# Performance work log

Measured on AMD Instinct MI355X. Metric: run time of the kernel, lower is better.

## Reference

```python
import jax, jax.numpy as jnp
import numpy as np

B = 16          # number of trees (batch)
H = 256         # hidden_size == feature_size
S = 16          # Tree.num_sem
C = 5           # max_child_num (complete C-ary tree)
L = 6           # tree depth: leaves at level L, internal levels 0..L-1
N_LEAF = C**L                     # 15625
N_INT = (C**L - 1) // (C - 1)     # 3906 internal nodes, level-l offset = (C^l-1)/(C-1)


def setup_inputs() -> dict:
    key = jax.random.key(0)
    ks = jax.random.split(key, 20)
    rn = lambda k, shp, s=0.05: jax.random.normal(k, shp, dtype=jnp.float32) * s
    return {
        "leaf_box": jax.random.normal(ks[0], (B, N_LEAF, 4), dtype=jnp.float32),
        "leaf_sem": jax.random.uniform(ks[1], (B, N_LEAF, S), dtype=jnp.float32),
        "internal_box": jax.random.normal(ks[2], (B, N_INT, 4), dtype=jnp.float32),
        "node_type": jax.random.randint(ks[3], (B, N_INT), 0, 3, dtype=jnp.int32),
        "eps": jax.random.normal(ks[4], (B, H), dtype=jnp.float32),
        "W_box": rn(ks[5], (4, H)), "b_box": jnp.zeros((H,), jnp.float32),
        "W_sem": rn(ks[6], (S, H)), "b_sem": jnp.zeros((H,), jnp.float32),
        "W_node": rn(ks[7], (3, C * H, H)), "b_node": jnp.zeros((3, H), jnp.float32),
        "W1": rn(ks[8], (H, H)), "b1": jnp.zeros((H,), jnp.float32),
        "Wmu": rn(ks[9], (H, H)), "bmu": jnp.zeros((H,), jnp.float32),
        "Wvar": rn(ks[10], (H, H)), "bvar": jnp.zeros((H,), jnp.float32),
    }


def reference(leaf_box, leaf_sem, internal_box, node_type, eps,
              W_box, b_box, W_sem, b_sem, W_node, b_node,
              W1, b1, Wmu, bmu, Wvar, bvar):
    box_enc = lambda b: jax.nn.relu(b @ W_box + b_box)
    # LeafEncoder: relu-box-encoding + relu-sem-encoding
    feats = box_enc(leaf_box) + jax.nn.relu(leaf_sem @ W_sem + b_sem)  # [B, N_LEAF, H]
    # Bottom-up over internal levels (static loop over L=6 levels)
    for l in range(L - 1, -1, -1):
        n = C ** l
        off = (C ** l - 1) // (C - 1)
        child = feats.reshape(B, n, C * H)  # children flattened per parent (child_exists==1)
        # Apply all 3 branch encoders (vertical/horizontal/stack), select by node label
        y_all = jnp.einsum('bnk,tkh->bnth', child, W_node) + b_node          # [B,n,3,H]
        sel = jax.nn.one_hot(node_type[:, off:off + n], 3, dtype=child.dtype)  # [B,n,3]
        y = jnp.einsum('bnth,bnt->bnh', y_all, sel)
        feats = jax.nn.relu(y) + box_enc(internal_box[:, off:off + n])
    root = feats[:, 0]  # [B, H]
    # Sampler (variational, probabilistic)
    enc = jax.nn.relu(root @ W1 + b1)
    mu = enc @ Wmu + bmu
    logvar = enc @ Wvar + bvar
    std = jnp.exp(0.5 * logvar)
    kld = 1.0 + logvar - mu ** 2 - jnp.exp(logvar)
    return jnp.concatenate([eps * std + mu, kld], axis=1)  # [B, 2H]
```

## Files before the change

kernel.cpp:

```cpp
#include <hip/hip_runtime.h>


#define B_ 16
#define H_ 256
#define NLEAF 15625
#define NINT 3906
#define RND128(x) (((x) + 127) & ~127)

typedef __bf16 bf16_t;
typedef bf16_t bf16x8 __attribute__((ext_vector_type(8)));
typedef bf16_t bf16x4 __attribute__((ext_vector_type(4)));
typedef float f32x4 __attribute__((ext_vector_type(4)));

__device__ __forceinline__ void gl2lds16(const bf16_t* g, bf16_t* l) {
  __builtin_amdgcn_global_load_lds((const __attribute__((address_space(1))) void*)g,
                                   (__attribute__((address_space(3))) void*)l,
                                   16, 0, 0);
}

__global__ __launch_bounds__(256) void prep_kernel(const float* __restrict__ W_node,
                                                   bf16_t* __restrict__ Wt,
                                                   int* __restrict__ counters) {
  if (blockIdx.x == 0 && threadIdx.x < 18) counters[threadIdx.x] = 0;
  const int t = blockIdx.x / 80;
  const int kc = blockIdx.x % 80;
  const int h = threadIdx.x;
  const int half = h >> 7, r = h & 127;
  const int sw = (r >> 1) & 3;
  const float* srcp = W_node + (size_t)t * 1280 * 256 + h;
  bf16_t* base = Wt + ((size_t)(t * 2 + half) * 40) * 4096 + r * 32;
#pragma unroll
  for (int k0 = kc * 16; k0 < kc * 16 + 16; k0 += 8) {
    bf16x8 v;
#pragma unroll
    for (int j = 0; j < 8; ++j) v[j] = (bf16_t)srcp[(size_t)(k0 + j) * 256];
    const int ks = k0 >> 5;
    const int q = (k0 >> 3) & 3;
    *(bf16x8*)(base + (size_t)ks * 4096 + ((q ^ sw) << 3)) = v;
  }
}

__global__ __launch_bounds__(256) void bucket_kernel(const int* __restrict__ node_type,
                                                     int* __restrict__ counters,
                                                     int2* __restrict__ buckets) {
  __shared__ int lcnt[18];
  __shared__ int lbase[18];
  const int tid = threadIdx.x;
  if (tid < 18) lcnt[tid] = 0;
  __syncthreads();

  int idx = blockIdx.x * 256 + tid;
  bool active = idx < B_ * NINT;
  int t = 0, key = 0, mypos = 0;
  int2 e;
  int base = 0, nl_cap = 0;
  if (active) {
    int b = idx / NINT;
    int j = idx - b * NINT;
    int l, off;
    if (j >= 781)      { l = 5; off = 781; }
    else if (j >= 156) { l = 4; off = 156; }
    else if (j >= 31)  { l = 3; off = 31; }
    else if (j >= 6)   { l = 2; off = 6; }
    else if (j >= 1)   { l = 1; off = 1; }
    else               { l = 0; off = 0; }
    const int n_tab[6]    = {1, 5, 25, 125, 625, 3125};
    const int nn_tab[6]   = {5, 25, 125, 625, 3125, 15625};
    const int base_tab[6] = {0, 48, 288, 1488, 7488, 37488};
    int n_l = n_tab[l], nn = nn_tab[l];
    t = node_type[idx];
    int i = j - off;
    e.x = b * n_l + i;
    e.y = b * nn + 5 * i;
    base = base_tab[l];
    nl_cap = B_ * n_l;
    key = l * 3 + t;
    mypos = atomicAdd(&lcnt[key], 1);
  }
  __syncthreads();
  if (tid < 18) {
    int c = lcnt[tid];
    lbase[tid] = c ? atomicAdd(&counters[tid], c) : 0;
  }
  __syncthreads();
  if (active) {
    buckets[base + t * nl_cap + lbase[key] + mypos] = e;
  }
}

__global__ __launch_bounds__(256) void dest_kernel(const int2* __restrict__ buckets,
                                                   const int* __restrict__ counters,
                                                   int* __restrict__ wdest_all,
                                                   int* __restrict__ rsrc6) {
  int flat = blockIdx.x * 256 + threadIdx.x;
  if (flat >= 187488) return;
  int l, base, cap, coff;
  if (flat >= 37488)      { l = 5; base = 37488; cap = 50000; coff = 0; }
  else if (flat >= 7488)  { l = 4; base = 7488;  cap = 10000; coff = 12480; }
  else if (flat >= 1488)  { l = 3; base = 1488;  cap = 2000;  coff = 2480; }
  else if (flat >= 288)   { l = 2; base = 288;   cap = 400;   coff = 480; }
  else if (flat >= 48)    { l = 1; base = 48;    cap = 80;    coff = 80; }
  else                    { l = 0; base = 0;     cap = 16;    coff = 0; }
  int rel = flat - base;
  int t = (rel >= 2 * cap) ? 2 : (rel >= cap ? 1 : 0);
  int s = rel - t * cap;
  const int* c3 = counters + l * 3;
  if (s >= c3[t]) return;
  int pfxr = (t > 0 ? RND128(c3[0]) : 0) + (t > 1 ? RND128(c3[1]) : 0);
  int R = pfxr + s;
  int2 e = buckets[flat];
  if (l == 5) {
    int* rp = rsrc6 + 5 * R;
#pragma unroll
    for (int c = 0; c < 5; ++c) rp[c] = e.y + c;
  } else {
    int* wp = wdest_all + coff + 5 * e.x;
#pragma unroll
    for (int c = 0; c < 5; ++c) wp[c] = (R << 3) + c;
  }
}

__global__ __launch_bounds__(256) void leaf_kernel(
    const float* __restrict__ leaf_box, const float* __restrict__ leaf_sem,
    const float* __restrict__ W_box, const float* __restrict__ b_box,
    const float* __restrict__ W_sem, const float* __restrict__ b_sem,
    const int* __restrict__ rsrc, bf16_t* __restrict__ g5) {
  const int lane = threadIdx.x & 63;
  const int wave = threadIdx.x >> 6;
  const int q = lane >> 4;
  const int c = lane & 15;
  const int hh = wave & 1;
  const int gw = wave >> 1;

  bf16x8 wsem[8], wbox[8];
#pragma unroll
  for (int T = 0; T < 8; ++T) {
    const int hb = (hh * 8 + T) * 16 + c;
    bf16x8 a;
#pragma unroll
    for (int j = 0; j < 8; ++j) a[j] = (bf16_t)0.f;
    if (q < 2) {
#pragma unroll
      for (int j = 0; j < 8; ++j) a[j] = (bf16_t)W_sem[(q * 8 + j) * H_ + hb];
    } else if (q == 2) {
      a[0] = (bf16_t)b_sem[hb];
    }
    wsem[T] = a;
    bf16x8 b;
#pragma unroll
    for (int j = 0; j < 8; ++j) b[j] = (bf16_t)0.f;
    if (q == 0) {
#pragma unroll
      for (int j = 0; j < 4; ++j) b[j] = (bf16_t)W_box[j * H_ + hb];
      b[4] = (bf16_t)b_box[hb];
    }
    wbox[T] = b;
  }

  const int NG2 = 15705;
  const int gstride = gridDim.x * 2;
  for (int g = blockIdx.x * 2 + gw; g < NG2; g += gstride) {
    const int ci = g * 16 + c;
    int row = rsrc[ci];
    row = ((unsigned)row < (unsigned)(B_ * NLEAF)) ? row : 0;
    const int R = ci / 5;
    const int c5 = ci - R * 5;
    bf16x8 xs, xb;
#pragma unroll
    for (int j = 0; j < 8; ++j) { xs[j] = (bf16_t)0.f; xb[j] = (bf16_t)0.f; }
    if (q < 2) {
      const float4* sp = (const float4*)(leaf_sem + (size_t)row * 16 + q * 8);
      float4 s0 = sp[0], s1 = sp[1];
      xs[0] = (bf16_t)s0.x; xs[1] = (bf16_t)s0.y; xs[2] = (bf16_t)s0.z; xs[3] = (bf16_t)s0.w;
      xs[4] = (bf16_t)s1.x; xs[5] = (bf16_t)s1.y; xs[6] = (bf16_t)s1.z; xs[7] = (bf16_t)s1.w;
    } else if (q == 2) {
      xs[0] = (bf16_t)1.0f;
    }
    if (q == 0) {
      float4 bx = *(const float4*)(leaf_box + (size_t)row * 4);
      xb[0] = (bf16_t)bx.x; xb[1] = (bf16_t)bx.y; xb[2] = (bf16_t)bx.z; xb[3] = (bf16_t)bx.w;
      xb[4] = (bf16_t)1.0f;
    }
    const int rr = R & 127;
    const int sw = (rr >> 1) & 3;
    bf16_t* obase = g5 + (size_t)(R >> 7) * 163840 + rr * 32;
#pragma unroll
    for (int T = 0; T < 8; ++T) {
      f32x4 z = {0.f, 0.f, 0.f, 0.f};
      f32x4 as = __builtin_amdgcn_mfma_f32_16x16x32_bf16(wsem[T], xs, z, 0, 0, 0);
      f32x4 ab = __builtin_amdgcn_mfma_f32_16x16x32_bf16(wbox[T], xb, z, 0, 0, 0);
      bf16x4 o;
#pragma unroll
      for (int r = 0; r < 4; ++r)
        o[r] = (bf16_t)(fmaxf(as[r], 0.f) + fmaxf(ab[r], 0.f));
      const int ks = c5 * 8 + hh * 4 + (T >> 1);
      const int pc = (((T & 1) << 1) | (q >> 1)) ^ sw;
      *(bf16x4*)(obase + (size_t)ks * 4096 + (pc << 3) + ((q & 1) << 2)) = o;
    }
  }
}

__global__ __launch_bounds__(256) void level_kernel(
    const bf16_t* __restrict__ src, bf16_t* __restrict__ dst,
    const int2* __restrict__ bucket, const int* __restrict__ counters,
    const bf16_t* __restrict__ Wt, const float* __restrict__ b_node,
    const float* __restrict__ ibox, const float* __restrict__ W_box,
    const float* __restrict__ b_box, const int* __restrict__ wdest,
    int n_l, int off_l, int cap) {
  const int t = blockIdx.y;
  const int cnt = counters[t];
  const int tile0 = blockIdx.x * 128;
  if (tile0 >= cnt) return;
  const int pfxr = (t > 0 ? RND128(counters[0]) : 0) + (t > 1 ? RND128(counters[1]) : 0);
  const int nblk = blockIdx.z;
  const int2* rd = bucket + (size_t)t * cap;

  __shared__ __align__(16) bf16_t Asm[3][128][32];
  __shared__ __align__(16) bf16_t Bsm[3][128][32];

  const int tid = threadIdx.x;
  const int lane = tid & 63;
  const int wave = tid >> 6;
  const int wm = wave & 1, wn = wave >> 1;
  const int quad = lane >> 4;
  const int l15 = lane & 15;

  const bf16_t* ga0 = src + (size_t)(pfxr + tile0) * 1280 + wave * 1024 + (lane << 3);
  const bf16_t* gb0 = Wt + ((size_t)(t * 2 + nblk) * 40) * 4096 + wave * 1024 + (lane << 3);

  f32x4 acc[4][4];
#pragma unroll
  for (int i = 0; i < 4; ++i)
#pragma unroll
    for (int j = 0; j < 4; ++j) acc[i][j] = (f32x4){0.f, 0.f, 0.f, 0.f};

  const int pcs = (quad ^ ((l15 >> 1) & 3)) * 8;

#define STAGE(buf, ks)                                  \
  {                                                     \
    const bf16_t* ga = ga0 + (ks) * 4096;               \
    const bf16_t* gb = gb0 + (ks) * 4096;               \
    bf16_t* la = &Asm[buf][0][0] + wave * 1024;         \
    bf16_t* lb = &Bsm[buf][0][0] + wave * 1024;         \
    gl2lds16(ga, la);                                   \
    gl2lds16(ga + 512, la + 512);                       \
    gl2lds16(gb, lb);                                   \
    gl2lds16(gb + 512, lb + 512);                       \
  }

#define FRAGS_AND_MFMA(bufv)                                                  \
  {                                                                           \
    bf16x8 af[4], bfr[4];                                                     \
    _Pragma("unroll") for (int am = 0; am < 4; ++am)                          \
        af[am] = *(const bf16x8*)(&Asm[bufv][wm * 64 + am * 16 + l15][pcs]);  \
    _Pragma("unroll") for (int bn = 0; bn < 4; ++bn)                          \
        bfr[bn] = *(const bf16x8*)(&Bsm[bufv][wn * 64 + bn * 16 + l15][pcs]); \
    __builtin_amdgcn_s_setprio(1);                                            \
    _Pragma("unroll") for (int am = 0; am < 4; ++am)                          \
        _Pragma("unroll") for (int bn = 0; bn < 4; ++bn)                      \
            acc[am][bn] = __builtin_amdgcn_mfma_f32_16x16x32_bf16(            \
                af[am], bfr[bn], acc[am][bn], 0, 0, 0);                       \
    __builtin_amdgcn_s_setprio(0);                                            \
  }

  STAGE(0, 0)
  STAGE(1, 1)
  int buf = 0, nxb = 2;
  for (int ks = 0; ks < 38; ++ks) {
    asm volatile("s_waitcnt vmcnt(4)" ::: "memory");
    __builtin_amdgcn_s_barrier();
    {
      bf16x8 af[4], bfr[4];
#pragma unroll
      for (int am = 0; am < 4; ++am)
        af[am] = *(const bf16x8*)(&Asm[buf][wm * 64 + am * 16 + l15][pcs]);
#pragma unroll
      for (int bn = 0; bn < 4; ++bn)
        bfr[bn] = *(const bf16x8*)(&Bsm[buf][wn * 64 + bn * 16 + l15][pcs]);
      STAGE(nxb, ks + 2)
      __builtin_amdgcn_s_setprio(1);
#pragma unroll
      for (int am = 0; am < 4; ++am)
#pragma unroll
        for (int bn = 0; bn < 4; ++bn)
          acc[am][bn] = __builtin_amdgcn_mfma_f32_16x16x32_bf16(af[am], bfr[bn], acc[am][bn], 0, 0, 0);
      __builtin_amdgcn_s_setprio(0);
    }
    buf = (buf == 2) ? 0 : buf + 1;
    nxb = (nxb == 2) ? 0 : nxb + 1;
  }
  asm volatile("s_waitcnt vmcnt(4)" ::: "memory");
  __builtin_amdgcn_s_barrier();
  FRAGS_AND_MFMA(buf)
  buf = (buf == 2) ? 0 : buf + 1;
  asm volatile("s_waitcnt vmcnt(0)" ::: "memory");
  __builtin_amdgcn_s_barrier();
  FRAGS_AND_MFMA(buf)
#undef FRAGS_AND_MFMA
#undef STAGE

  float wbv[4][6];
#pragma unroll
  for (int bn = 0; bn < 4; ++bn) {
    int col = nblk * 128 + wn * 64 + bn * 16 + l15;
    wbv[bn][0] = W_box[col];
    wbv[bn][1] = W_box[H_ + col];
    wbv[bn][2] = W_box[2 * H_ + col];
    wbv[bn][3] = W_box[3 * H_ + col];
    wbv[bn][4] = b_box[col];
    wbv[bn][5] = b_node[t * H_ + col];
  }
#pragma unroll
  for (int am = 0; am < 4; ++am) {
    int orw_[4]; float4 bxv[4]; bool valid[4];
#pragma unroll
    for (int r = 0; r < 4; ++r) {
      int gidx = tile0 + wm * 64 + am * 16 + quad * 4 + r;
      valid[r] = (gidx < cnt);
      int ic = valid[r] ? gidx : (cnt - 1);
      int orw = rd[ic].x;
      orw_[r] = orw;
      int b = orw / n_l;
      int i = orw - b * n_l;
      bxv[r] = *(const float4*)(ibox + ((size_t)b * NINT + off_l + i) * 4);
    }
    if (wdest) {
      size_t ob[4]; int sw_[4];
#pragma unroll
      for (int r = 0; r < 4; ++r) {
        int wd = wdest[orw_[r]];
        int R = wd >> 3, cc = wd & 7;
        int rr = R & 127;
        ob[r] = (size_t)(R >> 7) * 163840 + (size_t)cc * 32768 + (size_t)rr * 32;
        sw_[r] = (rr >> 1) & 3;
      }
#pragma unroll
      for (int bn = 0; bn < 4; ++bn) {
        int col = nblk * 128 + wn * 64 + bn * 16 + l15;
        int kc2 = col >> 5, qq = (col >> 3) & 3, ww = col & 7;
#pragma unroll
        for (int r = 0; r < 4; ++r) {
          if (!valid[r]) continue;
          float y = fmaxf(acc[am][bn][r] + wbv[bn][5], 0.f);
          float be = fmaf(wbv[bn][0], bxv[r].x,
                     fmaf(wbv[bn][1], bxv[r].y,
                     fmaf(wbv[bn][2], bxv[r].z,
                     fmaf(wbv[bn][3], bxv[r].w, wbv[bn][4]))));
          be = fmaxf(be, 0.f);
          dst[ob[r] + (size_t)kc2 * 4096 + ((qq ^ sw_[r]) << 3) + ww] = (bf16_t)(y + be);
        }
      }
    } else {
#pragma unroll
      for (int bn = 0; bn < 4; ++bn) {
        int col = nblk * 128 + wn * 64 + bn * 16 + l15;
#pragma unroll
        for (int r = 0; r < 4; ++r) {
          if (!valid[r]) continue;
          float y = fmaxf(acc[am][bn][r] + wbv[bn][5], 0.f);
          float be = fmaf(wbv[bn][0], bxv[r].x,
                     fmaf(wbv[bn][1], bxv[r].y,
                     fmaf(wbv[bn][2], bxv[r].z,
                     fmaf(wbv[bn][3], bxv[r].w, wbv[bn][4]))));
          be = fmaxf(be, 0.f);
          dst[(size_t)orw_[r] * H_ + col] = (bf16_t)(y + be);
        }
      }
    }
  }
}

__global__ __launch_bounds__(256) void head_kernel(
    const bf16_t* __restrict__ f0, const float* __restrict__ eps,
    const float* __restrict__ W1, const float* __restrict__ b1,
    const float* __restrict__ Wmu, const float* __restrict__ bmu,
    const float* __restrict__ Wvar, const float* __restrict__ bvar,
    float* __restrict__ out) {
  __shared__ float root[256];
  __shared__ float enc[256];
  int b = blockIdx.x, h = threadIdx.x;
  root[h] = (float)f0[b * H_ + h];
  __syncthreads();
  float a = b1[h];
  for (int k = 0; k < 256; ++k) a = fmaf(root[k], W1[k * H_ + h], a);
  enc[h] = fmaxf(a, 0.f);
  __syncthreads();
  float m = bmu[h], lv = bvar[h];
  for (int k = 0; k < 256; ++k) {
    float e = enc[k];
    m = fmaf(e, Wmu[k * H_ + h], m);
    lv = fmaf(e, Wvar[k * H_ + h], lv);
  }
  float stdv = expf(0.5f * lv);
  float kld = 1.f + lv - m * m - expf(lv);
  out[b * 512 + h] = eps[b * H_ + h] * stdv + m;
  out[b * 512 + 256 + h] = kld;
}

extern "C" void kernel_launch(void* const* d_in, const int* in_sizes, int n_in,
                              void* d_out, int out_size, void* d_ws, size_t ws_size,
                              hipStream_t stream) {
  const float* leaf_box     = (const float*)d_in[0];
  const float* leaf_sem     = (const float*)d_in[1];
  const float* internal_box = (const float*)d_in[2];
  const int*   node_type    = (const int*)d_in[3];
  const float* eps          = (const float*)d_in[4];
  const float* W_box        = (const float*)d_in[5];
  const float* b_box        = (const float*)d_in[6];
  const float* W_sem        = (const float*)d_in[7];
  const float* b_sem        = (const float*)d_in[8];
  const float* W_node       = (const float*)d_in[9];
  const float* b_node       = (const float*)d_in[10];
  const float* W1           = (const float*)d_in[11];
  const float* b1           = (const float*)d_in[12];
  const float* Wmu          = (const float*)d_in[13];
  const float* bmu          = (const float*)d_in[14];
  const float* Wvar         = (const float*)d_in[15];
  const float* bvar         = (const float*)d_in[16];
  float* out = (float*)d_out;

  char* p = (char*)d_ws;
  auto alloc = [&](size_t bytes) {
    char* r = p;
    p += (bytes + 255) & ~(size_t)255;
    return r;
  };
  const int n_tab[6] = {1, 5, 25, 125, 625, 3125};
  bf16_t* Wt = (bf16_t*)alloc((size_t)3 * 2 * 40 * 4096 * 2);
  bf16_t* f0 = (bf16_t*)alloc((size_t)B_ * H_ * 2);
  bf16_t* G[6];
  for (int l = 0; l <= 5; ++l)
    G[l] = (bf16_t*)alloc(((size_t)B_ * n_tab[l] + 384) * 1280 * 2);
  int* counters  = (int*)alloc(18 * 4);
  int2* buckets  = (int2*)alloc((size_t)187488 * 8);
  int* wdest_all = (int*)alloc((size_t)62480 * 4);
  int* rsrc6     = (int*)alloc((size_t)251280 * 4);

  hipLaunchKernelGGL(prep_kernel, dim3(240), dim3(256), 0, stream, W_node, Wt, counters);
  hipLaunchKernelGGL(bucket_kernel, dim3((B_ * NINT + 255) / 256), dim3(256), 0, stream,
                     node_type, counters, buckets);
  hipLaunchKernelGGL(dest_kernel, dim3((187488 + 255) / 256), dim3(256), 0, stream,
                     buckets, counters, wdest_all, rsrc6);
  hipLaunchKernelGGL(leaf_kernel, dim3(1024), dim3(256), 0, stream,
                     leaf_box, leaf_sem, W_box, b_box, W_sem, b_sem, rsrc6, G[5]);

  const int lvl_base[6] = {0, 48, 288, 1488, 7488, 37488};
  const int off_tab[6]  = {0, 1, 6, 31, 156, 781};
  const int woff[6]     = {0, 0, 80, 480, 2480, 12480};
  for (int l = 5; l >= 0; --l) {
    int cap = B_ * n_tab[l];
    int tiles = (cap + 127) / 128;
    const int* wdp = (l >= 1) ? (wdest_all + woff[l]) : nullptr;
    hipLaunchKernelGGL(level_kernel, dim3(tiles, 3, 2), dim3(256), 0, stream,
                       G[l], (l >= 1) ? G[l - 1] : f0, buckets + lvl_base[l],
                       counters + l * 3, Wt, b_node, internal_box, W_box, b_box,
                       wdp, n_tab[l], off_tab[l], cap);
  }
  hipLaunchKernelGGL(head_kernel, dim3(16), dim3(256), 0, stream,
                     f0, eps, W1, b1, Wmu, bmu, Wvar, bvar, out);
}
```

Baseline: 373.5 us.

## Template level kernel on prefetch depth and interleave N-blocks in grid

The level GEMM kernel gains a pipeline-depth template parameter: level 5 keeps a 2-stage prefetch, and the smaller levels use 4 stages in flight with matching vmcnt waits and a peeled tail. The grid also folds the two N-halves into blockIdx.x, interleaving them in groups of 8 tiles so blocks that share the same A rows launch close together and can reuse them in cache. Deeper buffering raises LDS use per block, which may lower occupancy.

```diff
diff --git a/kernel.cpp b/kernel.cpp
--- a/kernel.cpp
+++ b/kernel.cpp
@@ -200,6 +200,7 @@
   }
 }
 
+template <int DEPTH>
 __global__ __launch_bounds__(256) void level_kernel(
     const bf16_t* __restrict__ src, bf16_t* __restrict__ dst,
     const int2* __restrict__ bucket, const int* __restrict__ counters,
@@ -207,16 +208,19 @@
     const float* __restrict__ ibox, const float* __restrict__ W_box,
     const float* __restrict__ b_box, const int* __restrict__ wdest,
     int n_l, int off_l, int cap) {
+  constexpr int NBUF = DEPTH + 1;
+  const int x = blockIdx.x;
+  const int p = ((x >> 4) << 3) + (x & 7);
+  const int nblk = (x >> 3) & 1;
   const int t = blockIdx.y;
   const int cnt = counters[t];
-  const int tile0 = blockIdx.x * 128;
+  const int tile0 = p * 128;
   if (tile0 >= cnt) return;
   const int pfxr = (t > 0 ? RND128(counters[0]) : 0) + (t > 1 ? RND128(counters[1]) : 0);
-  const int nblk = blockIdx.z;
   const int2* rd = bucket + (size_t)t * cap;
 
-  __shared__ __align__(16) bf16_t Asm[3][128][32];
-  __shared__ __align__(16) bf16_t Bsm[3][128][32];
+  __shared__ __align__(16) bf16_t Asm[NBUF][128][32];
+  __shared__ __align__(16) bf16_t Bsm[NBUF][128][32];
 
   const int tid = threadIdx.x;
   const int lane = tid & 63;
@@ -263,21 +267,22 @@
     __builtin_amdgcn_s_setprio(0);                                            \
   }
 
-  STAGE(0, 0)
-  STAGE(1, 1)
-  int buf = 0, nxb = 2;
-  for (int ks = 0; ks < 38; ++ks) {
-    asm volatile("s_waitcnt vmcnt(4)" ::: "memory");
+#pragma unroll
+  for (int i = 0; i < DEPTH; ++i) STAGE(i, i)
+  int rbuf = 0, wbuf = DEPTH;
+  for (int ks = 0; ks < 40 - DEPTH; ++ks) {
+    if constexpr (DEPTH == 2) asm volatile("s_waitcnt vmcnt(4)" ::: "memory");
+    else                      asm volatile("s_waitcnt vmcnt(12)" ::: "memory");
     __builtin_amdgcn_s_barrier();
     {
       bf16x8 af[4], bfr[4];
 #pragma unroll
       for (int am = 0; am < 4; ++am)
-        af[am] = *(const bf16x8*)(&Asm[buf][wm * 64 + am * 16 + l15][pcs]);
+        af[am] = *(const bf16x8*)(&Asm[rbuf][wm * 64 + am * 16 + l15][pcs]);
 #pragma unroll
       for (int bn = 0; bn < 4; ++bn)
-        bfr[bn] = *(const bf16x8*)(&Bsm[buf][wn * 64 + bn * 16 + l15][pcs]);
-      STAGE(nxb, ks + 2)
+        bfr[bn] = *(const bf16x8*)(&Bsm[rbuf][wn * 64 + bn * 16 + l15][pcs]);
+      STAGE(wbuf, ks + DEPTH)
       __builtin_amdgcn_s_setprio(1);
 #pragma unroll
       for (int am = 0; am < 4; ++am)
@@ -286,16 +291,17 @@
           acc[am][bn] = __builtin_amdgcn_mfma_f32_16x16x32_bf16(af[am], bfr[bn], acc[am][bn], 0, 0, 0);
       __builtin_amdgcn_s_setprio(0);
     }
-    buf = (buf == 2) ? 0 : buf + 1;
-    nxb = (nxb == 2) ? 0 : nxb + 1;
-  }
-  asm volatile("s_waitcnt vmcnt(4)" ::: "memory");
-  __builtin_amdgcn_s_barrier();
-  FRAGS_AND_MFMA(buf)
-  buf = (buf == 2) ? 0 : buf + 1;
-  asm volatile("s_waitcnt vmcnt(0)" ::: "memory");
-  __builtin_amdgcn_s_barrier();
-  FRAGS_AND_MFMA(buf)
+    rbuf = (rbuf + 1 == NBUF) ? 0 : rbuf + 1;
+    wbuf = (wbuf + 1 == NBUF) ? 0 : wbuf + 1;
+  }
+#define PEEL(N)                                           \
+  asm volatile("s_waitcnt vmcnt(" #N ")" ::: "memory");   \
+  __builtin_amdgcn_s_barrier();                           \
+  FRAGS_AND_MFMA(rbuf)                                    \
+  rbuf = (rbuf + 1 == NBUF) ? 0 : rbuf + 1;
+  if constexpr (DEPTH == 4) { PEEL(12) PEEL(8) PEEL(4) PEEL(0) }
+  else                      { PEEL(4) PEEL(0) }
+#undef PEEL
 #undef FRAGS_AND_MFMA
 #undef STAGE
 
@@ -450,11 +456,20 @@
   for (int l = 5; l >= 0; --l) {
     int cap = B_ * n_tab[l];
     int tiles = (cap + 127) / 128;
+    int tiles8 = (tiles + 7) & ~7;
+    dim3 grid(2 * tiles8, 3);
     const int* wdp = (l >= 1) ? (wdest_all + woff[l]) : nullptr;
-    hipLaunchKernelGGL(level_kernel, dim3(tiles, 3, 2), dim3(256), 0, stream,
-                       G[l], (l >= 1) ? G[l - 1] : f0, buckets + lvl_base[l],
-                       counters + l * 3, Wt, b_node, internal_box, W_box, b_box,
-                       wdp, n_tab[l], off_tab[l], cap);
+    bf16_t* dstp = (l >= 1) ? G[l - 1] : f0;
+    if (l == 5)
+      hipLaunchKernelGGL(HIP_KERNEL_NAME(level_kernel<2>), grid, dim3(256), 0, stream,
+                         G[l], dstp, buckets + lvl_base[l], counters + l * 3,
+                         Wt, b_node, internal_box, W_box, b_box, wdp,
+                         n_tab[l], off_tab[l], cap);
+    else
+      hipLaunchKernelGGL(HIP_KERNEL_NAME(level_kernel<4>), grid, dim3(256), 0, stream,
+                         G[l], dstp, buckets + lvl_base[l], counters + l * 3,
+                         Wt, b_node, internal_box, W_box, b_box, wdp,
+                         n_tab[l], off_tab[l], cap);
   }
   hipLaunchKernelGGL(head_kernel, dim3(16), dim3(256), 0, stream,
                      f0, eps, W1, b1, Wmu, bmu, Wvar, bvar, out);
```

After: 373.8 us. About the same (+0.1%).

## Fuse upper tree levels and head into persistent kernel with grid barriers

Applied to the files above, without the earlier changes.

Levels 4..0 and the VAE head now run in one persistent kernel of 474 blocks, with software grid barriers (atomic counters) between levels instead of six separate kernel launches. The largest level gets its own kernel whose block index is remapped so the two N-halves of a tile run near each other, which may improve L2 reuse of the A tiles. This removes launch gaps and tail latency on the small levels. In exchange it relies on all 474 blocks being co-resident (launch_bounds 2 per CU), and the spin-wait barriers add their own overhead.

```diff
diff --git a/kernel.cpp b/kernel.cpp
--- a/kernel.cpp
+++ b/kernel.cpp
@@ -6,6 +6,7 @@
 #define NLEAF 15625
 #define NINT 3906
 #define RND128(x) (((x) + 127) & ~127)
+#define MEGA_NBLK 474
 
 typedef __bf16 bf16_t;
 typedef bf16_t bf16x8 __attribute__((ext_vector_type(8)));
@@ -21,7 +22,7 @@
 __global__ __launch_bounds__(256) void prep_kernel(const float* __restrict__ W_node,
                                                    bf16_t* __restrict__ Wt,
                                                    int* __restrict__ counters) {
-  if (blockIdx.x == 0 && threadIdx.x < 18) counters[threadIdx.x] = 0;
+  if (blockIdx.x == 0 && threadIdx.x < 24) counters[threadIdx.x] = 0;
   const int t = blockIdx.x / 80;
   const int kc = blockIdx.x % 80;
   const int h = threadIdx.x;
@@ -200,23 +201,24 @@
   }
 }
 
-__global__ __launch_bounds__(256) void level_kernel(
-    const bf16_t* __restrict__ src, bf16_t* __restrict__ dst,
+__device__ __forceinline__ void level_phase(
+    int x, const bf16_t* __restrict__ src, bf16_t* __restrict__ dst,
     const int2* __restrict__ bucket, const int* __restrict__ counters,
     const bf16_t* __restrict__ Wt, const float* __restrict__ b_node,
     const float* __restrict__ ibox, const float* __restrict__ W_box,
     const float* __restrict__ b_box, const int* __restrict__ wdest,
-    int n_l, int off_l, int cap) {
-  const int t = blockIdx.y;
+    int n_l, int off_l, int cap, int P,
+    bf16_t Asm[3][128][32], bf16_t Bsm[3][128][32]) {
+  if (x >= 6 * P) return;
+  const int t = x / (2 * P);
+  const int r2 = x - t * 2 * P;
+  const int nblk = r2 / P;
+  const int p = r2 - nblk * P;
   const int cnt = counters[t];
-  const int tile0 = blockIdx.x * 128;
+  const int tile0 = p * 128;
   if (tile0 >= cnt) return;
   const int pfxr = (t > 0 ? RND128(counters[0]) : 0) + (t > 1 ? RND128(counters[1]) : 0);
-  const int nblk = blockIdx.z;
   const int2* rd = bucket + (size_t)t * cap;
-
-  __shared__ __align__(16) bf16_t Asm[3][128][32];
-  __shared__ __align__(16) bf16_t Bsm[3][128][32];
 
   const int tid = threadIdx.x;
   const int lane = tid & 63;
@@ -236,7 +238,7 @@
 
   const int pcs = (quad ^ ((l15 >> 1) & 3)) * 8;
 
-#define STAGE(buf, ks)                                  \
+#define STG2(buf, ks)                                   \
   {                                                     \
     const bf16_t* ga = ga0 + (ks) * 4096;               \
     const bf16_t* gb = gb0 + (ks) * 4096;               \
@@ -247,8 +249,7 @@
     gl2lds16(gb, lb);                                   \
     gl2lds16(gb + 512, lb + 512);                       \
   }
-
-#define FRAGS_AND_MFMA(bufv)                                                  \
+#define FRG2(bufv)                                                            \
   {                                                                           \
     bf16x8 af[4], bfr[4];                                                     \
     _Pragma("unroll") for (int am = 0; am < 4; ++am)                          \
@@ -263,9 +264,9 @@
     __builtin_amdgcn_s_setprio(0);                                            \
   }
 
-  STAGE(0, 0)
-  STAGE(1, 1)
-  int buf = 0, nxb = 2;
+  STG2(0, 0)
+  STG2(1, 1)
+  int rbuf = 0, wbuf = 2;
   for (int ks = 0; ks < 38; ++ks) {
     asm volatile("s_waitcnt vmcnt(4)" ::: "memory");
     __builtin_amdgcn_s_barrier();
@@ -273,11 +274,11 @@
       bf16x8 af[4], bfr[4];
 #pragma unroll
       for (int am = 0; am < 4; ++am)
-        af[am] = *(const bf16x8*)(&Asm[buf][wm * 64 + am * 16 + l15][pcs]);
+        af[am] = *(const bf16x8*)(&Asm[rbuf][wm * 64 + am * 16 + l15][pcs]);
 #pragma unroll
       for (int bn = 0; bn < 4; ++bn)
-        bfr[bn] = *(const bf16x8*)(&Bsm[buf][wn * 64 + bn * 16 + l15][pcs]);
-      STAGE(nxb, ks + 2)
+        bfr[bn] = *(const bf16x8*)(&Bsm[rbuf][wn * 64 + bn * 16 + l15][pcs]);
+      STG2(wbuf, ks + 2)
       __builtin_amdgcn_s_setprio(1);
 #pragma unroll
       for (int am = 0; am < 4; ++am)
@@ -286,18 +287,18 @@
           acc[am][bn] = __builtin_amdgcn_mfma_f32_16x16x32_bf16(af[am], bfr[bn], acc[am][bn], 0, 0, 0);
       __builtin_amdgcn_s_setprio(0);
     }
-    buf = (buf == 2) ? 0 : buf + 1;
-    nxb = (nxb == 2) ? 0 : nxb + 1;
+    rbuf = (rbuf + 1 == 3) ? 0 : rbuf + 1;
+    wbuf = (wbuf + 1 == 3) ? 0 : wbuf + 1;
   }
   asm volatile("s_waitcnt vmcnt(4)" ::: "memory");
   __builtin_amdgcn_s_barrier();
-  FRAGS_AND_MFMA(buf)
-  buf = (buf == 2) ? 0 : buf + 1;
+  FRG2(rbuf)
+  rbuf = (rbuf + 1 == 3) ? 0 : rbuf + 1;
   asm volatile("s_waitcnt vmcnt(0)" ::: "memory");
   __builtin_amdgcn_s_barrier();
-  FRAGS_AND_MFMA(buf)
-#undef FRAGS_AND_MFMA
-#undef STAGE
+  FRG2(rbuf)
+#undef FRG2
+#undef STG2
 
   float wbv[4][6];
 #pragma unroll
@@ -370,31 +371,100 @@
   }
 }
 
-__global__ __launch_bounds__(256) void head_kernel(
-    const bf16_t* __restrict__ f0, const float* __restrict__ eps,
-    const float* __restrict__ W1, const float* __restrict__ b1,
-    const float* __restrict__ Wmu, const float* __restrict__ bmu,
-    const float* __restrict__ Wvar, const float* __restrict__ bvar,
-    float* __restrict__ out) {
-  __shared__ float root[256];
-  __shared__ float enc[256];
-  int b = blockIdx.x, h = threadIdx.x;
-  root[h] = (float)f0[b * H_ + h];
+__global__ __launch_bounds__(256) void level5_kernel(
+    const bf16_t* __restrict__ src, bf16_t* __restrict__ dst,
+    const int2* __restrict__ bucket, const int* __restrict__ counters,
+    const bf16_t* __restrict__ Wt, const float* __restrict__ b_node,
+    const float* __restrict__ ibox, const float* __restrict__ W_box,
+    const float* __restrict__ b_box, const int* __restrict__ wdest,
+    int n_l, int off_l, int cap) {
+  __shared__ __align__(16) bf16_t Asm[3][128][32];
+  __shared__ __align__(16) bf16_t Bsm[3][128][32];
+  const int x = blockIdx.x;
+  const int p = ((x >> 4) << 3) + (x & 7);
+  const int nblk = (x >> 3) & 1;
+  const int t = blockIdx.y;
+  const int P = gridDim.x / 2;
+  const int xx = t * 2 * P + nblk * P + p;
+  level_phase(xx, src, dst, bucket, counters, Wt, b_node, ibox, W_box, b_box,
+              wdest, n_l, off_l, cap, P, Asm, Bsm);
+}
+
+__device__ __forceinline__ void grid_barrier(int* bar, int ph) {
   __syncthreads();
-  float a = b1[h];
-  for (int k = 0; k < 256; ++k) a = fmaf(root[k], W1[k * H_ + h], a);
-  enc[h] = fmaxf(a, 0.f);
+  if (threadIdx.x == 0) {
+    __threadfence();
+    __hip_atomic_fetch_add(&bar[ph], 1, __ATOMIC_RELEASE, __HIP_MEMORY_SCOPE_AGENT);
+    while (__hip_atomic_load(&bar[ph], __ATOMIC_ACQUIRE, __HIP_MEMORY_SCOPE_AGENT) < MEGA_NBLK)
+      __builtin_amdgcn_s_sleep(2);
+    __threadfence();
+  }
   __syncthreads();
-  float m = bmu[h], lv = bvar[h];
-  for (int k = 0; k < 256; ++k) {
-    float e = enc[k];
-    m = fmaf(e, Wmu[k * H_ + h], m);
-    lv = fmaf(e, Wvar[k * H_ + h], lv);
-  }
-  float stdv = expf(0.5f * lv);
-  float kld = 1.f + lv - m * m - expf(lv);
-  out[b * 512 + h] = eps[b * H_ + h] * stdv + m;
-  out[b * 512 + 256 + h] = kld;
+}
+
+struct MegaArgs {
+  const bf16_t* src[5];
+  bf16_t* dst[5];
+  const int2* buckets;
+  const int* counters;
+  int* bar;
+  const int* wdest_all;
+  const bf16_t* Wt;
+  const float* b_node;
+  const float* ibox;
+  const float* W_box;
+  const float* b_box;
+  const bf16_t* f0;
+  const float* eps;
+  const float* W1;
+  const float* b1;
+  const float* Wmu;
+  const float* bmu;
+  const float* Wvar;
+  const float* bvar;
+  float* out;
+};
+
+__global__ __launch_bounds__(256, 2) void mega_kernel(MegaArgs a) {
+  __shared__ __align__(16) bf16_t Asm[3][128][32];
+  __shared__ __align__(16) bf16_t Bsm[3][128][32];
+  __shared__ float hroot[256];
+  __shared__ float henc[256];
+  constexpr int BKT_OFF[5] = {7488, 1488, 288, 48, 0};
+  constexpr int CNT_OFF[5] = {12, 9, 6, 3, 0};
+  constexpr int WOFF[5]    = {2480, 480, 80, 0, -1};
+  constexpr int NL[5]      = {625, 125, 25, 5, 1};
+  constexpr int OFFL[5]    = {156, 31, 6, 1, 0};
+  constexpr int CAP[5]     = {10000, 2000, 400, 80, 16};
+  constexpr int PAIRS[5]   = {79, 16, 4, 1, 1};
+  const int x = blockIdx.x;
+#pragma unroll
+  for (int li = 0; li < 5; ++li) {
+    const int* wd = (li == 4) ? nullptr : (a.wdest_all + WOFF[li]);
+    level_phase(x, a.src[li], a.dst[li], a.buckets + BKT_OFF[li],
+                a.counters + CNT_OFF[li], a.Wt, a.b_node, a.ibox, a.W_box,
+                a.b_box, wd, NL[li], OFFL[li], CAP[li], PAIRS[li], Asm, Bsm);
+    grid_barrier(a.bar, li);
+  }
+  if (blockIdx.x < 16) {
+    const int b = blockIdx.x, h = threadIdx.x;
+    hroot[h] = (float)a.f0[b * H_ + h];
+    __syncthreads();
+    float v = a.b1[h];
+    for (int k = 0; k < 256; ++k) v = fmaf(hroot[k], a.W1[k * H_ + h], v);
+    henc[h] = fmaxf(v, 0.f);
+    __syncthreads();
+    float m = a.bmu[h], lv = a.bvar[h];
+    for (int k = 0; k < 256; ++k) {
+      float e = henc[k];
+      m = fmaf(e, a.Wmu[k * H_ + h], m);
+      lv = fmaf(e, a.Wvar[k * H_ + h], lv);
+    }
+    float stdv = expf(0.5f * lv);
+    float kld = 1.f + lv - m * m - expf(lv);
+    a.out[b * 512 + h] = a.eps[b * H_ + h] * stdv + m;
+    a.out[b * 512 + 256 + h] = kld;
+  }
 }
 
 extern "C" void kernel_launch(void* const* d_in, const int* in_sizes, int n_in,
@@ -431,7 +501,7 @@
   bf16_t* G[6];
   for (int l = 0; l <= 5; ++l)
     G[l] = (bf16_t*)alloc(((size_t)B_ * n_tab[l] + 384) * 1280 * 2);
-  int* counters  = (int*)alloc(18 * 4);
+  int* counters  = (int*)alloc(32 * 4);
   int2* buckets  = (int2*)alloc((size_t)187488 * 8);
   int* wdest_all = (int*)alloc((size_t)62480 * 4);
   int* rsrc6     = (int*)alloc((size_t)251280 * 4);
@@ -444,18 +514,29 @@
   hipLaunchKernelGGL(leaf_kernel, dim3(1024), dim3(256), 0, stream,
                      leaf_box, leaf_sem, W_box, b_box, W_sem, b_sem, rsrc6, G[5]);
 
-  const int lvl_base[6] = {0, 48, 288, 1488, 7488, 37488};
-  const int off_tab[6]  = {0, 1, 6, 31, 156, 781};
-  const int woff[6]     = {0, 0, 80, 480, 2480, 12480};
-  for (int l = 5; l >= 0; --l) {
-    int cap = B_ * n_tab[l];
+  {
+    int cap = B_ * n_tab[5];
     int tiles = (cap + 127) / 128;
-    const int* wdp = (l >= 1) ? (wdest_all + woff[l]) : nullptr;
-    hipLaunchKernelGGL(level_kernel, dim3(tiles, 3, 2), dim3(256), 0, stream,
-                       G[l], (l >= 1) ? G[l - 1] : f0, buckets + lvl_base[l],
-                       counters + l * 3, Wt, b_node, internal_box, W_box, b_box,
-                       wdp, n_tab[l], off_tab[l], cap);
-  }
-  hipLaunchKernelGGL(head_kernel, dim3(16), dim3(256), 0, stream,
-                     f0, eps, W1, b1, Wmu, bmu, Wvar, bvar, out);
-}
+    int tiles8 = (tiles + 7) & ~7;
+    hipLaunchKernelGGL(level5_kernel, dim3(2 * tiles8, 3), dim3(256), 0, stream,
+                       G[5], G[4], buckets + 37488, counters + 15,
+                       Wt, b_node, internal_box, W_box, b_box,
+                       wdest_all + 12480, 3125, 781, cap);
+  }
+
+  {
+    MegaArgs ma;
+    ma.src[0] = G[4]; ma.dst[0] = G[3];
+    ma.src[1] = G[3]; ma.dst[1] = G[2];
+    ma.src[2] = G[2]; ma.dst[2] = G[1];
+    ma.src[3] = G[1]; ma.dst[3] = G[0];
+    ma.src[4] = G[0]; ma.dst[4] = f0;
+    ma.buckets = buckets; ma.counters = counters; ma.bar = counters + 18;
+    ma.wdest_all = wdest_all;
+    ma.Wt = Wt; ma.b_node = b_node; ma.ibox = internal_box;
+    ma.W_box = W_box; ma.b_box = b_box;
+    ma.f0 = f0; ma.eps = eps; ma.W1 = W1; ma.b1 = b1;
+    ma.Wmu = Wmu; ma.bmu = bmu; ma.Wvar = Wvar; ma.bvar = bvar; ma.out = out;
+    hipLaunchKernelGGL(mega_kernel, dim3(MEGA_NBLK), dim3(256), 0, stream, ma);
+  }
+}
```

Measured after the change: 1.205 ms. 223% more time.

## Add skinny direct-load level kernel for small levels and remap level-5 block order

Applied to the files above, without the earlier changes.

Level 5 now runs through a wrapper kernel that remaps block indices so that groups of 8 row-tiles alternate between the two N halves, improving L2 reuse of the shared A tiles. Levels 4 to 0 use a new kernel that processes 16-row tiles across the full 256 columns, loading operands straight from global memory into registers with no LDS staging or barriers. This creates many more small blocks on the sparse upper levels, where 128-row tiles would mostly idle, at the cost of lower data reuse per block.

```diff
diff --git a/kernel.cpp b/kernel.cpp
--- a/kernel.cpp
+++ b/kernel.cpp
@@ -200,23 +200,24 @@
   }
 }
 
-__global__ __launch_bounds__(256) void level_kernel(
-    const bf16_t* __restrict__ src, bf16_t* __restrict__ dst,
+__device__ __forceinline__ void level_phase(
+    int x, const bf16_t* __restrict__ src, bf16_t* __restrict__ dst,
     const int2* __restrict__ bucket, const int* __restrict__ counters,
     const bf16_t* __restrict__ Wt, const float* __restrict__ b_node,
     const float* __restrict__ ibox, const float* __restrict__ W_box,
     const float* __restrict__ b_box, const int* __restrict__ wdest,
-    int n_l, int off_l, int cap) {
-  const int t = blockIdx.y;
+    int n_l, int off_l, int cap, int P,
+    bf16_t Asm[3][128][32], bf16_t Bsm[3][128][32]) {
+  if (x >= 6 * P) return;
+  const int t = x / (2 * P);
+  const int r2 = x - t * 2 * P;
+  const int nblk = r2 / P;
+  const int p = r2 - nblk * P;
   const int cnt = counters[t];
-  const int tile0 = blockIdx.x * 128;
+  const int tile0 = p * 128;
   if (tile0 >= cnt) return;
   const int pfxr = (t > 0 ? RND128(counters[0]) : 0) + (t > 1 ? RND128(counters[1]) : 0);
-  const int nblk = blockIdx.z;
   const int2* rd = bucket + (size_t)t * cap;
-
-  __shared__ __align__(16) bf16_t Asm[3][128][32];
-  __shared__ __align__(16) bf16_t Bsm[3][128][32];
 
   const int tid = threadIdx.x;
   const int lane = tid & 63;
@@ -236,7 +237,7 @@
 
   const int pcs = (quad ^ ((l15 >> 1) & 3)) * 8;
 
-#define STAGE(buf, ks)                                  \
+#define STG2(buf, ks)                                   \
   {                                                     \
     const bf16_t* ga = ga0 + (ks) * 4096;               \
     const bf16_t* gb = gb0 + (ks) * 4096;               \
@@ -247,8 +248,7 @@
     gl2lds16(gb, lb);                                   \
     gl2lds16(gb + 512, lb + 512);                       \
   }
-
-#define FRAGS_AND_MFMA(bufv)                                                  \
+#define FRG2(bufv)                                                            \
   {                                                                           \
     bf16x8 af[4], bfr[4];                                                     \
     _Pragma("unroll") for (int am = 0; am < 4; ++am)                          \
@@ -263,9 +263,9 @@
     __builtin_amdgcn_s_setprio(0);                                            \
   }
 
-  STAGE(0, 0)
-  STAGE(1, 1)
-  int buf = 0, nxb = 2;
+  STG2(0, 0)
+  STG2(1, 1)
+  int rbuf = 0, wbuf = 2;
   for (int ks = 0; ks < 38; ++ks) {
     asm volatile("s_waitcnt vmcnt(4)" ::: "memory");
     __builtin_amdgcn_s_barrier();
@@ -273,11 +273,11 @@
       bf16x8 af[4], bfr[4];
 #pragma unroll
       for (int am = 0; am < 4; ++am)
-        af[am] = *(const bf16x8*)(&Asm[buf][wm * 64 + am * 16 + l15][pcs]);
+        af[am] = *(const bf16x8*)(&Asm[rbuf][wm * 64 + am * 16 + l15][pcs]);
 #pragma unroll
       for (int bn = 0; bn < 4; ++bn)
-        bfr[bn] = *(const bf16x8*)(&Bsm[buf][wn * 64 + bn * 16 + l15][pcs]);
-      STAGE(nxb, ks + 2)
+        bfr[bn] = *(const bf16x8*)(&Bsm[rbuf][wn * 64 + bn * 16 + l15][pcs]);
+      STG2(wbuf, ks + 2)
       __builtin_amdgcn_s_setprio(1);
 #pragma unroll
       for (int am = 0; am < 4; ++am)
@@ -286,18 +286,18 @@
           acc[am][bn] = __builtin_amdgcn_mfma_f32_16x16x32_bf16(af[am], bfr[bn], acc[am][bn], 0, 0, 0);
       __builtin_amdgcn_s_setprio(0);
     }
-    buf = (buf == 2) ? 0 : buf + 1;
-    nxb = (nxb == 2) ? 0 : nxb + 1;
+    rbuf = (rbuf + 1 == 3) ? 0 : rbuf + 1;
+    wbuf = (wbuf + 1 == 3) ? 0 : wbuf + 1;
   }
   asm volatile("s_waitcnt vmcnt(4)" ::: "memory");
   __builtin_amdgcn_s_barrier();
-  FRAGS_AND_MFMA(buf)
-  buf = (buf == 2) ? 0 : buf + 1;
+  FRG2(rbuf)
+  rbuf = (rbuf + 1 == 3) ? 0 : rbuf + 1;
   asm volatile("s_waitcnt vmcnt(0)" ::: "memory");
   __builtin_amdgcn_s_barrier();
-  FRAGS_AND_MFMA(buf)
-#undef FRAGS_AND_MFMA
-#undef STAGE
+  FRG2(rbuf)
+#undef FRG2
+#undef STG2
 
   float wbv[4][6];
 #pragma unroll
@@ -365,6 +365,144 @@
           be = fmaxf(be, 0.f);
           dst[(size_t)orw_[r] * H_ + col] = (bf16_t)(y + be);
         }
+      }
+    }
+  }
+}
+
+__global__ __launch_bounds__(256) void level5_kernel(
+    const bf16_t* __restrict__ src, bf16_t* __restrict__ dst,
+    const int2* __restrict__ bucket, const int* __restrict__ counters,
+    const bf16_t* __restrict__ Wt, const float* __restrict__ b_node,
+    const float* __restrict__ ibox, const float* __restrict__ W_box,
+    const float* __restrict__ b_box, const int* __restrict__ wdest,
+    int n_l, int off_l, int cap) {
+  __shared__ __align__(16) bf16_t Asm[3][128][32];
+  __shared__ __align__(16) bf16_t Bsm[3][128][32];
+  const int x = blockIdx.x;
+  const int p = ((x >> 4) << 3) + (x & 7);
+  const int nblk = (x >> 3) & 1;
+  const int t = blockIdx.y;
+  const int P = gridDim.x / 2;
+  const int xx = t * 2 * P + nblk * P + p;
+  level_phase(xx, src, dst, bucket, counters, Wt, b_node, ibox, W_box, b_box,
+              wdest, n_l, off_l, cap, P, Asm, Bsm);
+}
+
+__global__ __launch_bounds__(256, 2) void level_direct(
+    const bf16_t* __restrict__ src, bf16_t* __restrict__ dst,
+    const int2* __restrict__ bucket, const int* __restrict__ counters,
+    const bf16_t* __restrict__ Wt, const float* __restrict__ b_node,
+    const float* __restrict__ ibox, const float* __restrict__ W_box,
+    const float* __restrict__ b_box, const int* __restrict__ wdest,
+    int n_l, int off_l, int cap, int TP) {
+  const int sl = blockIdx.x;
+  const int t = sl / TP;
+  const int s = sl - t * TP;
+  const int cnt = counters[t];
+  const int tile0 = s * 16;
+  if (tile0 >= cnt) return;
+  const int pfxr = (t > 0 ? RND128(counters[0]) : 0) + (t > 1 ? RND128(counters[1]) : 0);
+  const int2* rd = bucket + (size_t)t * cap;
+
+  const int tid = threadIdx.x;
+  const int lane = tid & 63;
+  const int wave = tid >> 6;
+  const int quad = lane >> 4;
+  const int l15 = lane & 15;
+  const int pcs = (quad ^ ((l15 >> 1) & 3)) * 8;
+
+  const int Rbase = pfxr + tile0;
+  const bf16_t* aptr = src + (size_t)(Rbase >> 7) * 163840 +
+                       ((Rbase & 127) + l15) * 32 + pcs;
+  const bf16_t* bptr[4];
+  int cols[4];
+#pragma unroll
+  for (int bn = 0; bn < 4; ++bn) {
+    int col = wave * 64 + bn * 16 + l15;
+    cols[bn] = col;
+    bptr[bn] = Wt + (size_t)(t * 2 + (col >> 7)) * 163840 + (col & 127) * 32 + pcs;
+  }
+
+  f32x4 acc[4];
+#pragma unroll
+  for (int bn = 0; bn < 4; ++bn) acc[bn] = (f32x4){0.f, 0.f, 0.f, 0.f};
+#pragma unroll
+  for (int g = 0; g < 10; ++g) {
+    bf16x8 af[4], b0[4], b1[4], b2[4], b3[4];
+#pragma unroll
+    for (int i = 0; i < 4; ++i) {
+      const size_t o = (size_t)(g * 4 + i) * 4096;
+      af[i] = *(const bf16x8*)(aptr + o);
+      b0[i] = *(const bf16x8*)(bptr[0] + o);
+      b1[i] = *(const bf16x8*)(bptr[1] + o);
+      b2[i] = *(const bf16x8*)(bptr[2] + o);
+      b3[i] = *(const bf16x8*)(bptr[3] + o);
+    }
+#pragma unroll
+    for (int i = 0; i < 4; ++i) {
+      acc[0] = __builtin_amdgcn_mfma_f32_16x16x32_bf16(af[i], b0[i], acc[0], 0, 0, 0);
+      acc[1] = __builtin_amdgcn_mfma_f32_16x16x32_bf16(af[i], b1[i], acc[1], 0, 0, 0);
+      acc[2] = __builtin_amdgcn_mfma_f32_16x16x32_bf16(af[i], b2[i], acc[2], 0, 0, 0);
+      acc[3] = __builtin_amdgcn_mfma_f32_16x16x32_bf16(af[i], b3[i], acc[3], 0, 0, 0);
+    }
+  }
+
+  int orw_[4]; float4 bxv[4]; bool valid[4];
+#pragma unroll
+  for (int r = 0; r < 4; ++r) {
+    int gidx = tile0 + quad * 4 + r;
+    valid[r] = (gidx < cnt);
+    int ic = valid[r] ? gidx : (cnt - 1);
+    int orw = rd[ic].x;
+    orw_[r] = orw;
+    int b = orw / n_l;
+    int i = orw - b * n_l;
+    bxv[r] = *(const float4*)(ibox + ((size_t)b * NINT + off_l + i) * 4);
+  }
+  if (wdest) {
+    size_t ob[4]; int swz[4];
+#pragma unroll
+    for (int r = 0; r < 4; ++r) {
+      int wd = wdest[orw_[r]];
+      int R = wd >> 3, cc = wd & 7;
+      int rr = R & 127;
+      ob[r] = (size_t)(R >> 7) * 163840 + (size_t)cc * 32768 + (size_t)rr * 32;
+      swz[r] = (rr >> 1) & 3;
+    }
+#pragma unroll
+    for (int bn = 0; bn < 4; ++bn) {
+      int col = cols[bn];
+      float w0 = W_box[col], w1 = W_box[H_ + col], w2 = W_box[2 * H_ + col];
+      float w3 = W_box[3 * H_ + col], w4 = b_box[col];
+      float bn5 = b_node[t * H_ + col];
+      int kc2 = col >> 5, qq = (col >> 3) & 3, ww = col & 7;
+#pragma unroll
+      for (int r = 0; r < 4; ++r) {
+        if (!valid[r]) continue;
+        float y = fmaxf(acc[bn][r] + bn5, 0.f);
+        float be = fmaf(w0, bxv[r].x, fmaf(w1, bxv[r].y,
+                   fmaf(w2, bxv[r].z, fmaf(w3, bxv[r].w, w4))));
+        be = fmaxf(be, 0.f);
+        dst[ob[r] + (size_t)kc2 * 4096 + ((size_t)(qq ^ swz[r]) << 3) + ww] =
+            (bf16_t)(y + be);
+      }
+    }
+  } else {
+#pragma unroll
+    for (int bn = 0; bn < 4; ++bn) {
+      int col = cols[bn];
+      float w0 = W_box[col], w1 = W_box[H_ + col], w2 = W_box[2 * H_ + col];
+      float w3 = W_box[3 * H_ + col], w4 = b_box[col];
+      float bn5 = b_node[t * H_ + col];
+#pragma unroll
+      for (int r = 0; r < 4; ++r) {
+        if (!valid[r]) continue;
+        float y = fmaxf(acc[bn][r] + bn5, 0.f);
+        float be = fmaf(w0, bxv[r].x, fmaf(w1, bxv[r].y,
+                   fmaf(w2, bxv[r].z, fmaf(w3, bxv[r].w, w4))));
+        be = fmaxf(be, 0.f);
+        dst[(size_t)orw_[r] * H_ + col] = (bf16_t)(y + be);
       }
     }
   }
@@ -431,7 +569,7 @@
   bf16_t* G[6];
   for (int l = 0; l <= 5; ++l)
     G[l] = (bf16_t*)alloc(((size_t)B_ * n_tab[l] + 384) * 1280 * 2);
-  int* counters  = (int*)alloc(18 * 4);
+  int* counters  = (int*)alloc(128 * 4);
   int2* buckets  = (int2*)alloc((size_t)187488 * 8);
   int* wdest_all = (int*)alloc((size_t)62480 * 4);
   int* rsrc6     = (int*)alloc((size_t)251280 * 4);
@@ -444,17 +582,27 @@
   hipLaunchKernelGGL(leaf_kernel, dim3(1024), dim3(256), 0, stream,
                      leaf_box, leaf_sem, W_box, b_box, W_sem, b_sem, rsrc6, G[5]);
 
+  {
+    int cap = B_ * n_tab[5];
+    int tiles = (cap + 127) / 128;
+    int tiles8 = (tiles + 7) & ~7;
+    hipLaunchKernelGGL(level5_kernel, dim3(2 * tiles8, 3), dim3(256), 0, stream,
+                       G[5], G[4], buckets + 37488, counters + 15,
+                       Wt, b_node, internal_box, W_box, b_box,
+                       wdest_all + 12480, 3125, 781, cap);
+  }
+
   const int lvl_base[6] = {0, 48, 288, 1488, 7488, 37488};
   const int off_tab[6]  = {0, 1, 6, 31, 156, 781};
   const int woff[6]     = {0, 0, 80, 480, 2480, 12480};
-  for (int l = 5; l >= 0; --l) {
-    int cap = B_ * n_tab[l];
-    int tiles = (cap + 127) / 128;
+  for (int l = 4; l >= 0; --l) {
+    int TP = n_tab[l];
     const int* wdp = (l >= 1) ? (wdest_all + woff[l]) : nullptr;
-    hipLaunchKernelGGL(level_kernel, dim3(tiles, 3, 2), dim3(256), 0, stream,
-                       G[l], (l >= 1) ? G[l - 1] : f0, buckets + lvl_base[l],
-                       counters + l * 3, Wt, b_node, internal_box, W_box, b_box,
-                       wdp, n_tab[l], off_tab[l], cap);
+    bf16_t* dstp = (l >= 1) ? G[l - 1] : f0;
+    hipLaunchKernelGGL(level_direct, dim3(3 * TP), dim3(256), 0, stream,
+                       G[l], dstp, buckets + lvl_base[l], counters + l * 3,
+                       Wt, b_node, internal_box, W_box, b_box, wdp,
+                       n_tab[l], off_tab[l], B_ * n_tab[l], TP);
   }
   hipLaunchKernelGGL(head_kernel, dim3(16), dim3(256), 0, stream,
                      f0, eps, W1, b1, Wmu, bmu, Wvar, bvar, out);
```

After: 349.0 us. -6.6%, faster.
